# Optimization experiments

Hardware: AMD Instinct MI355X
Metric: run time of the kernel (lower is better)

Reference implementation:

```python
import jax, jax.numpy as jnp
import numpy as np

B, LE, LD = 8, 4096, 4096
DE, DD, A = 512, 512, 128


def setup_inputs() -> dict:
    key = jax.random.key(0)
    ks = jax.random.split(key, 9)
    f32 = jnp.float32
    return {
        "encoder_outputs": jax.random.normal(ks[0], (B, LE, DE), f32),
        "decoder_outputs": jax.random.normal(ks[1], (B, LD, DD), f32),
        # linear_q / linear_k / linear_v (Dense with bias, relu activation)
        "Wq": jax.random.normal(ks[2], (DD, A), f32) * 0.05,
        "bq": jnp.zeros((A,), f32),
        "Wk": jax.random.normal(ks[3], (DE, A), f32) * 0.05,
        "bk": jnp.zeros((A,), f32),
        "Wv": jax.random.normal(ks[4], (DE, A), f32) * 0.05,
        "bv": jnp.zeros((A,), f32),
        # perceptron branch weights (Dense, no bias)
        "Pw": jax.random.normal(ks[5], (A, A), f32) * 0.05,
        "Pu": jax.random.normal(ks[6], (A, A), f32) * 0.05,
        "pv": jax.random.normal(ks[7], (A, 1), f32) * 0.05,
    }


def reference(encoder_outputs, decoder_outputs, Wq, bq, Wk, bk, Wv, bv, Pw, Pu, pv):
    att = Wq.shape[1]
    q = jax.nn.relu(decoder_outputs @ Wq + bq)   # [B, Ld, A]
    k = jax.nn.relu(encoder_outputs @ Wk + bk)   # [B, Le, A]
    v = jax.nn.relu(encoder_outputs @ Wv + bv)   # [B, Le, A]
    # perceptron score: pv^T (Pw q_i + Pu k_j). No nonlinearity between the
    # sum and pv, so it decomposes additively -> no [B,Ld,Le,A] tiling needed.
    q_term = (q @ Pw) @ pv                        # [B, Ld, 1]
    k_term = (k @ Pu) @ pv                        # [B, Le, 1]
    scores = (q_term + jnp.swapaxes(k_term, 1, 2)) / jnp.sqrt(jnp.float32(att))  # [B, Ld, Le]
    weights = jax.nn.softmax(scores, axis=-1)
    attention = jnp.einsum('bij,bjd->bid', weights, v)  # [B, Ld, A]
    return attention
```

## Files before the change

kernel.cpp:

```cpp
#include <hip/hip_runtime.h>
#include <hip/hip_bf16.h>

#define B_   8
#define LE_  4096
#define LD_  4096
#define DE_  512
#define AA_  128
#define RTOT (B_*LE_)
#define NDIM 256
#define KDIM 512
#define BM   64
#define BK   64
#define LDSS 72

typedef __attribute__((ext_vector_type(8))) short short8;
typedef __attribute__((ext_vector_type(4))) float f32x4;

#define WCT_OFF   0
#define U_OFF     262144
#define BIAS_OFF  262656
#define NUM_OFF   263680
#define RS_OFF    267776
#define KT_OFF    267840
#define WW_OFF    398912
#define C_OFF     529984

__device__ inline ushort f2bf(float f) {
    union { float f; unsigned u; } x; x.f = f;
    unsigned r = x.u + 0x7fffu + ((x.u >> 16) & 1u);
    return (ushort)(r >> 16);
}

__global__ void prep_kernel(const float* __restrict__ Wk, const float* __restrict__ bk,
                            const float* __restrict__ Wv, const float* __restrict__ bv,
                            const float* __restrict__ Pu, const float* __restrict__ pv,
                            ushort* __restrict__ wct, float* __restrict__ u,
                            float* __restrict__ bias, float* __restrict__ num) {
    int t = threadIdx.x;
    int base = blockIdx.x * 256 + t;
    for (int i = 0; i < 4; ++i) {
        int idx = base + i * 32768;
        int n = idx >> 9, k = idx & 511;
        float s = (n < 128) ? Wk[k * 128 + n] : Wv[k * 128 + (n - 128)];
        wct[idx] = f2bf(s);
    }
    if (blockIdx.x == 0) {
        if (t < 128) {
            float acc = 0.f;
            for (int c = 0; c < 128; ++c) acc += Pu[t * 128 + c] * pv[c];
            u[t] = acc;
        }
        bias[t] = (t < 128) ? bk[t] : bv[t - 128];
        for (int i = 0; i < 4; ++i) num[t + i * 256] = 0.f;
    }
}

__global__ __launch_bounds__(256)
void gemm_kernel(const float* __restrict__ enc, const ushort* __restrict__ wct,
                 const float* __restrict__ bias, float* __restrict__ C) {
    __shared__ ushort As[BM][LDSS];
    __shared__ ushort Bs[NDIM][LDSS];
    const int t = threadIdx.x;
    const int wv = t >> 6, l = t & 63;
    const int m = l & 15, kb = l >> 4;
    const int row0 = blockIdx.x * BM;

    f32x4 acc[4][4] = {};

    for (int k0 = 0; k0 < KDIM; k0 += BK) {
#pragma unroll
        for (int i = 0; i < 2; ++i) {
            int c = t + i * 256;
            int r = c >> 3, k8 = (c & 7) * 8;
            const float4* src = (const float4*)(enc + (size_t)(row0 + r) * KDIM + k0 + k8);
            float4 a0 = src[0], a1 = src[1];
            int4 pk;
            pk.x = (int)f2bf(a0.x) | ((int)f2bf(a0.y) << 16);
            pk.y = (int)f2bf(a0.z) | ((int)f2bf(a0.w) << 16);
            pk.z = (int)f2bf(a1.x) | ((int)f2bf(a1.y) << 16);
            pk.w = (int)f2bf(a1.z) | ((int)f2bf(a1.w) << 16);
            *(int4*)&As[r][k8] = pk;
        }
#pragma unroll
        for (int i = 0; i < 8; ++i) {
            int c = t + i * 256;
            int n = c >> 3, k8 = (c & 7) * 8;
            int4 v = *(const int4*)(wct + (size_t)n * KDIM + k0 + k8);
            *(int4*)&Bs[n][k8] = v;
        }
        __syncthreads();
#pragma unroll
        for (int kc = 0; kc < 2; ++kc) {
            short8 afr[4], bfr[4];
#pragma unroll
            for (int mt = 0; mt < 4; ++mt)
                afr[mt] = *(const short8*)&As[mt * 16 + m][kc * 32 + kb * 8];
#pragma unroll
            for (int nt = 0; nt < 4; ++nt)
                bfr[nt] = *(const short8*)&Bs[wv * 64 + nt * 16 + m][kc * 32 + kb * 8];
#pragma unroll
            for (int mt = 0; mt < 4; ++mt)
#pragma unroll
                for (int nt = 0; nt < 4; ++nt)
                    acc[mt][nt] = __builtin_amdgcn_mfma_f32_16x16x32_bf16(
                        afr[mt], bfr[nt], acc[mt][nt], 0, 0, 0);
        }
        __syncthreads();
    }
    const int rgrp = l >> 4;
#pragma unroll
    for (int mt = 0; mt < 4; ++mt) {
#pragma unroll
        for (int nt = 0; nt < 4; ++nt) {
            int col = wv * 64 + nt * 16 + (l & 15);
            float bsv = bias[col];
#pragma unroll
            for (int r = 0; r < 4; ++r) {
                int rowl = mt * 16 + rgrp * 4 + r;
                float v = acc[mt][nt][r] + bsv;
                C[(size_t)(row0 + rowl) * NDIM + col] = v > 0.f ? v : 0.f;
            }
        }
    }
}

__global__ void kt_kernel(const float* __restrict__ C, const float* __restrict__ u,
                          float* __restrict__ kt) {
    int gid = blockIdx.x * 256 + threadIdx.x;
    int r = gid >> 6, l = gid & 63;
    float a = C[(size_t)r * NDIM + l] * u[l] + C[(size_t)r * NDIM + 64 + l] * u[64 + l];
#pragma unroll
    for (int off = 32; off > 0; off >>= 1) a += __shfl_down(a, off);
    if (l == 0) kt[r] = a;
}

__global__ __launch_bounds__(1024)
void softmax_kernel(const float* __restrict__ kt, float* __restrict__ w,
                    float* __restrict__ rS) {
    __shared__ float red[1024];
    int b = blockIdx.x, t = threadIdx.x;
    const float inv_s = 0.08838834764831843f;
    float v[4], m = -1e30f;
#pragma unroll
    for (int i = 0; i < 4; ++i) {
        v[i] = kt[b * 4096 + i * 1024 + t];
        m = fmaxf(m, v[i]);
    }
    red[t] = m; __syncthreads();
    for (int off = 512; off > 0; off >>= 1) {
        if (t < off) red[t] = fmaxf(red[t], red[t + off]);
        __syncthreads();
    }
    float M = red[0]; __syncthreads();
    float s = 0.f;
#pragma unroll
    for (int i = 0; i < 4; ++i) {
        float e = __expf((v[i] - M) * inv_s);
        w[b * 4096 + i * 1024 + t] = e;
        s += e;
    }
    red[t] = s; __syncthreads();
    for (int off = 512; off > 0; off >>= 1) {
        if (t < off) red[t] += red[t + off];
        __syncthreads();
    }
    if (t == 0) rS[b] = 1.0f / red[0];
}

__global__ void wsum_kernel(const float* __restrict__ C, const float* __restrict__ w,
                            float* __restrict__ num) {
    int b = blockIdx.x >> 4, ch = blockIdx.x & 15;
    int t = threadIdx.x;
    int d = t & 127, jj = t >> 7;
    size_t base_row = (size_t)b * 4096 + ch * 256;
    float acc = 0.f;
    for (int j = jj; j < 256; j += 2) {
        size_t r = base_row + j;
        acc += w[r] * C[r * NDIM + 128 + d];
    }
    atomicAdd(&num[b * 128 + d], acc);
}

__global__ void bcast_kernel(const float* __restrict__ num, const float* __restrict__ rS,
                             float4* __restrict__ out) {
    int g = blockIdx.x * 256 + threadIdx.x;
    const float4* n4 = (const float4*)num;
    const int total4 = B_ * LD_ * AA_ / 4;
    for (int c = g; c < total4; c += 262144) {
        int flat = c * 4;
        int b = flat >> 19;
        int d = flat & 127;
        float4 nv = n4[b * 32 + (d >> 2)];
        float s = rS[b];
        float4 o;
        o.x = nv.x * s; o.y = nv.y * s; o.z = nv.z * s; o.w = nv.w * s;
        out[c] = o;
    }
}

extern "C" void kernel_launch(void* const* d_in, const int* in_sizes, int n_in,
                              void* d_out, int out_size, void* d_ws, size_t ws_size,
                              hipStream_t stream) {
    const float* enc = (const float*)d_in[0];
    const float* Wk = (const float*)d_in[4];
    const float* bk = (const float*)d_in[5];
    const float* Wv = (const float*)d_in[6];
    const float* bv = (const float*)d_in[7];
    const float* Pu = (const float*)d_in[9];
    const float* pv = (const float*)d_in[10];

    char* ws = (char*)d_ws;
    ushort* wct  = (ushort*)(ws + WCT_OFF);
    float*  u    = (float*)(ws + U_OFF);
    float*  bias = (float*)(ws + BIAS_OFF);
    float*  num  = (float*)(ws + NUM_OFF);
    float*  rS   = (float*)(ws + RS_OFF);
    float*  kt   = (float*)(ws + KT_OFF);
    float*  w    = (float*)(ws + WW_OFF);
    float*  C    = (float*)(ws + C_OFF);

    prep_kernel<<<128, 256, 0, stream>>>(Wk, bk, Wv, bv, Pu, pv, wct, u, bias, num);
    gemm_kernel<<<RTOT / BM, 256, 0, stream>>>(enc, wct, bias, C);
    kt_kernel<<<RTOT / 4, 256, 0, stream>>>(C, u, kt);
    softmax_kernel<<<B_, 1024, 0, stream>>>(kt, w, rS);
    wsum_kernel<<<B_ * 16, 256, 0, stream>>>(C, w, num);
    bcast_kernel<<<1024, 256, 0, stream>>>(num, rS, (float4*)d_out);
}
```

Measured before the change: 214.0 us.

## Fuse key-score reduction into GEMM epilogue and store V as bf16

The GEMM now runs 512 threads per block with a 2x4 wave split. Its epilogue computes the k·u score directly using shuffle and LDS reductions, and writes only the V half, in bf16. This removes the kt kernel and the full fp32 C buffer round-trip through memory. Softmax now uses wave shuffles, normalizes the weights itself, and drops the separate reciprocal. wsum reads bf16 V with vectorized loads, and bcast becomes a pure copy. The cost is lower precision in V, which is rounded to bf16 before the weighted sum.

```diff
diff --git a/kernel.cpp b/kernel.cpp
--- a/kernel.cpp
+++ b/kernel.cpp
@@ -4,14 +4,10 @@
 #define B_   8
 #define LE_  4096
 #define LD_  4096
-#define DE_  512
+#define KDIM 512
 #define AA_  128
 #define RTOT (B_*LE_)
 #define NDIM 256
-#define KDIM 512
-#define BM   64
-#define BK   64
-#define LDSS 72
 
 typedef __attribute__((ext_vector_type(8))) short short8;
 typedef __attribute__((ext_vector_type(4))) float f32x4;
@@ -20,15 +16,18 @@
 #define U_OFF     262144
 #define BIAS_OFF  262656
 #define NUM_OFF   263680
-#define RS_OFF    267776
-#define KT_OFF    267840
-#define WW_OFF    398912
-#define C_OFF     529984
+#define S_OFF     267776
+#define WN_OFF    398848
+#define VB_OFF    529920
 
 __device__ inline ushort f2bf(float f) {
     union { float f; unsigned u; } x; x.f = f;
     unsigned r = x.u + 0x7fffu + ((x.u >> 16) & 1u);
     return (ushort)(r >> 16);
+}
+__device__ inline float bf2f(ushort s) {
+    union { unsigned u; float f; } x; x.u = ((unsigned)s) << 16;
+    return x.f;
 }
 
 __global__ void prep_kernel(const float* __restrict__ Wk, const float* __restrict__ bk,
@@ -55,23 +54,24 @@
     }
 }
 
-__global__ __launch_bounds__(256)
-void gemm_kernel(const float* __restrict__ enc, const ushort* __restrict__ wct,
-                 const float* __restrict__ bias, float* __restrict__ C) {
-    __shared__ ushort As[BM][LDSS];
-    __shared__ ushort Bs[NDIM][LDSS];
+__global__ __launch_bounds__(512, 4)
+void gemm_fused(const float* __restrict__ enc, const ushort* __restrict__ wct,
+                const float* __restrict__ bias, const float* __restrict__ u,
+                ushort* __restrict__ vbuf, float* __restrict__ sout) {
+    __shared__ ushort As[64][72];
+    __shared__ ushort Bs[256][72];
+    __shared__ float s_red[64][2];
     const int t = threadIdx.x;
     const int wv = t >> 6, l = t & 63;
+    const int wm = wv >> 2, wn = wv & 3;
     const int m = l & 15, kb = l >> 4;
-    const int row0 = blockIdx.x * BM;
-
-    f32x4 acc[4][4] = {};
-
-    for (int k0 = 0; k0 < KDIM; k0 += BK) {
-#pragma unroll
-        for (int i = 0; i < 2; ++i) {
-            int c = t + i * 256;
-            int r = c >> 3, k8 = (c & 7) * 8;
+    const int row0 = blockIdx.x * 64;
+
+    f32x4 acc[2][4] = {};
+
+    for (int k0 = 0; k0 < KDIM; k0 += 64) {
+        {
+            int r = t >> 3, k8 = (t & 7) * 8;
             const float4* src = (const float4*)(enc + (size_t)(row0 + r) * KDIM + k0 + k8);
             float4 a0 = src[0], a1 = src[1];
             int4 pk;
@@ -82,24 +82,23 @@
             *(int4*)&As[r][k8] = pk;
         }
 #pragma unroll
-        for (int i = 0; i < 8; ++i) {
-            int c = t + i * 256;
+        for (int i = 0; i < 4; ++i) {
+            int c = t + i * 512;
             int n = c >> 3, k8 = (c & 7) * 8;
-            int4 v = *(const int4*)(wct + (size_t)n * KDIM + k0 + k8);
-            *(int4*)&Bs[n][k8] = v;
+            *(int4*)&Bs[n][k8] = *(const int4*)(wct + (size_t)n * KDIM + k0 + k8);
         }
         __syncthreads();
 #pragma unroll
         for (int kc = 0; kc < 2; ++kc) {
-            short8 afr[4], bfr[4];
-#pragma unroll
-            for (int mt = 0; mt < 4; ++mt)
-                afr[mt] = *(const short8*)&As[mt * 16 + m][kc * 32 + kb * 8];
+            short8 afr[2], bfr[4];
+#pragma unroll
+            for (int mt = 0; mt < 2; ++mt)
+                afr[mt] = *(const short8*)&As[wm * 32 + mt * 16 + m][kc * 32 + kb * 8];
 #pragma unroll
             for (int nt = 0; nt < 4; ++nt)
-                bfr[nt] = *(const short8*)&Bs[wv * 64 + nt * 16 + m][kc * 32 + kb * 8];
-#pragma unroll
-            for (int mt = 0; mt < 4; ++mt)
+                bfr[nt] = *(const short8*)&Bs[wn * 64 + nt * 16 + m][kc * 32 + kb * 8];
+#pragma unroll
+            for (int mt = 0; mt < 2; ++mt)
 #pragma unroll
                 for (int nt = 0; nt < 4; ++nt)
                     acc[mt][nt] = __builtin_amdgcn_mfma_f32_16x16x32_bf16(
@@ -107,94 +106,141 @@
         }
         __syncthreads();
     }
-    const int rgrp = l >> 4;
-#pragma unroll
-    for (int mt = 0; mt < 4; ++mt) {
-#pragma unroll
-        for (int nt = 0; nt < 4; ++nt) {
-            int col = wv * 64 + nt * 16 + (l & 15);
-            float bsv = bias[col];
-#pragma unroll
-            for (int r = 0; r < 4; ++r) {
-                int rowl = mt * 16 + rgrp * 4 + r;
-                float v = acc[mt][nt][r] + bsv;
-                C[(size_t)(row0 + rowl) * NDIM + col] = v > 0.f ? v : 0.f;
-            }
-        }
-    }
-}
-
-__global__ void kt_kernel(const float* __restrict__ C, const float* __restrict__ u,
-                          float* __restrict__ kt) {
-    int gid = blockIdx.x * 256 + threadIdx.x;
-    int r = gid >> 6, l = gid & 63;
-    float a = C[(size_t)r * NDIM + l] * u[l] + C[(size_t)r * NDIM + 64 + l] * u[64 + l];
-#pragma unroll
-    for (int off = 32; off > 0; off >>= 1) a += __shfl_down(a, off);
-    if (l == 0) kt[r] = a;
+
+    const int rg = l >> 4;
+    if (wn >= 2) {
+#pragma unroll
+        for (int mt = 0; mt < 2; ++mt) {
+#pragma unroll
+            for (int nt = 0; nt < 4; ++nt) {
+                int col = wn * 64 + nt * 16 + m;
+                float bsv = bias[col];
+#pragma unroll
+                for (int j = 0; j < 4; ++j) {
+                    int rowl = wm * 32 + mt * 16 + rg * 4 + j;
+                    float v = acc[mt][nt][j] + bsv;
+                    v = v > 0.f ? v : 0.f;
+                    vbuf[(size_t)(row0 + rowl) * AA_ + (col - 128)] = f2bf(v);
+                }
+            }
+        }
+    } else {
+#pragma unroll
+        for (int mt = 0; mt < 2; ++mt) {
+            float p[4] = {0.f, 0.f, 0.f, 0.f};
+#pragma unroll
+            for (int nt = 0; nt < 4; ++nt) {
+                int col = wn * 64 + nt * 16 + m;
+                float bsv = bias[col];
+                float uw = u[col];
+#pragma unroll
+                for (int j = 0; j < 4; ++j) {
+                    float v = acc[mt][nt][j] + bsv;
+                    v = v > 0.f ? v : 0.f;
+                    p[j] += v * uw;
+                }
+            }
+#pragma unroll
+            for (int j = 0; j < 4; ++j) {
+                p[j] += __shfl_xor(p[j], 1);
+                p[j] += __shfl_xor(p[j], 2);
+                p[j] += __shfl_xor(p[j], 4);
+                p[j] += __shfl_xor(p[j], 8);
+            }
+            if (m == 0) {
+#pragma unroll
+                for (int j = 0; j < 4; ++j)
+                    s_red[wm * 32 + mt * 16 + rg * 4 + j][wn] = p[j];
+            }
+        }
+    }
+    __syncthreads();
+    if (t < 64) sout[row0 + t] = s_red[t][0] + s_red[t][1];
 }
 
 __global__ __launch_bounds__(1024)
-void softmax_kernel(const float* __restrict__ kt, float* __restrict__ w,
-                    float* __restrict__ rS) {
-    __shared__ float red[1024];
+void softmax_kernel(const float* __restrict__ s, float* __restrict__ wnorm) {
+    __shared__ float red[17];
     int b = blockIdx.x, t = threadIdx.x;
+    int l = t & 63, wv = t >> 6;
     const float inv_s = 0.08838834764831843f;
     float v[4], m = -1e30f;
 #pragma unroll
     for (int i = 0; i < 4; ++i) {
-        v[i] = kt[b * 4096 + i * 1024 + t];
+        v[i] = s[b * 4096 + i * 1024 + t];
         m = fmaxf(m, v[i]);
     }
-    red[t] = m; __syncthreads();
-    for (int off = 512; off > 0; off >>= 1) {
-        if (t < off) red[t] = fmaxf(red[t], red[t + off]);
-        __syncthreads();
-    }
-    float M = red[0]; __syncthreads();
-    float s = 0.f;
+#pragma unroll
+    for (int off = 1; off < 64; off <<= 1) m = fmaxf(m, __shfl_xor(m, off));
+    if (l == 0) red[wv] = m;
+    __syncthreads();
+    if (t == 0) {
+        float x = red[0];
+        for (int i = 1; i < 16; ++i) x = fmaxf(x, red[i]);
+        red[16] = x;
+    }
+    __syncthreads();
+    float M = red[16];
+    __syncthreads();
+    float e[4], sum = 0.f;
 #pragma unroll
     for (int i = 0; i < 4; ++i) {
-        float e = __expf((v[i] - M) * inv_s);
-        w[b * 4096 + i * 1024 + t] = e;
-        s += e;
-    }
-    red[t] = s; __syncthreads();
-    for (int off = 512; off > 0; off >>= 1) {
-        if (t < off) red[t] += red[t + off];
-        __syncthreads();
-    }
-    if (t == 0) rS[b] = 1.0f / red[0];
-}
-
-__global__ void wsum_kernel(const float* __restrict__ C, const float* __restrict__ w,
-                            float* __restrict__ num) {
-    int b = blockIdx.x >> 4, ch = blockIdx.x & 15;
-    int t = threadIdx.x;
-    int d = t & 127, jj = t >> 7;
-    size_t base_row = (size_t)b * 4096 + ch * 256;
-    float acc = 0.f;
-    for (int j = jj; j < 256; j += 2) {
-        size_t r = base_row + j;
-        acc += w[r] * C[r * NDIM + 128 + d];
-    }
-    atomicAdd(&num[b * 128 + d], acc);
-}
-
-__global__ void bcast_kernel(const float* __restrict__ num, const float* __restrict__ rS,
-                             float4* __restrict__ out) {
+        e[i] = __expf((v[i] - M) * inv_s);
+        sum += e[i];
+    }
+#pragma unroll
+    for (int off = 1; off < 64; off <<= 1) sum += __shfl_xor(sum, off);
+    if (l == 0) red[wv] = sum;
+    __syncthreads();
+    if (t == 0) {
+        float x = 0.f;
+        for (int i = 0; i < 16; ++i) x += red[i];
+        red[16] = 1.0f / x;
+    }
+    __syncthreads();
+    float rS = red[16];
+#pragma unroll
+    for (int i = 0; i < 4; ++i)
+        wnorm[b * 4096 + i * 1024 + t] = e[i] * rS;
+}
+
+__global__ __launch_bounds__(256)
+void wsum_kernel(const ushort* __restrict__ vbuf, const float* __restrict__ wnorm,
+                 float* __restrict__ num) {
+    int b = blockIdx.x >> 3, ch = blockIdx.x & 7;
+    int t = threadIdx.x, wv = t >> 6, l = t & 63;
+    int rg = l >> 4, d8 = (l & 15) * 8;
+    int rbase = b * 4096 + ch * 512;
+    float acc[8] = {};
+    for (int it = 0; it < 32; ++it) {
+        int r = rbase + it * 16 + wv * 4 + rg;
+        float wj = wnorm[r];
+        short8 vv = *(const short8*)(vbuf + (size_t)r * AA_ + d8);
+#pragma unroll
+        for (int j = 0; j < 8; ++j)
+            acc[j] += wj * bf2f((ushort)vv[j]);
+    }
+#pragma unroll
+    for (int j = 0; j < 8; ++j) {
+        acc[j] += __shfl_xor(acc[j], 16);
+        acc[j] += __shfl_xor(acc[j], 32);
+    }
+    if (l < 16) {
+#pragma unroll
+        for (int j = 0; j < 8; ++j)
+            atomicAdd(&num[b * AA_ + d8 + j], acc[j]);
+    }
+}
+
+__global__ void bcast_kernel(const float* __restrict__ num, float4* __restrict__ out) {
     int g = blockIdx.x * 256 + threadIdx.x;
     const float4* n4 = (const float4*)num;
     const int total4 = B_ * LD_ * AA_ / 4;
-    for (int c = g; c < total4; c += 262144) {
+    for (int c = g; c < total4; c += 524288) {
         int flat = c * 4;
         int b = flat >> 19;
         int d = flat & 127;
-        float4 nv = n4[b * 32 + (d >> 2)];
-        float s = rS[b];
-        float4 o;
-        o.x = nv.x * s; o.y = nv.y * s; o.z = nv.z * s; o.w = nv.w * s;
-        out[c] = o;
+        out[c] = n4[b * 32 + (d >> 2)];
     }
 }
 
@@ -210,19 +256,17 @@
     const float* pv = (const float*)d_in[10];
 
     char* ws = (char*)d_ws;
-    ushort* wct  = (ushort*)(ws + WCT_OFF);
-    float*  u    = (float*)(ws + U_OFF);
-    float*  bias = (float*)(ws + BIAS_OFF);
-    float*  num  = (float*)(ws + NUM_OFF);
-    float*  rS   = (float*)(ws + RS_OFF);
-    float*  kt   = (float*)(ws + KT_OFF);
-    float*  w    = (float*)(ws + WW_OFF);
-    float*  C    = (float*)(ws + C_OFF);
+    ushort* wct   = (ushort*)(ws + WCT_OFF);
+    float*  u     = (float*)(ws + U_OFF);
+    float*  bias  = (float*)(ws + BIAS_OFF);
+    float*  num   = (float*)(ws + NUM_OFF);
+    float*  s     = (float*)(ws + S_OFF);
+    float*  wnorm = (float*)(ws + WN_OFF);
+    ushort* vbuf  = (ushort*)(ws + VB_OFF);
 
     prep_kernel<<<128, 256, 0, stream>>>(Wk, bk, Wv, bv, Pu, pv, wct, u, bias, num);
-    gemm_kernel<<<RTOT / BM, 256, 0, stream>>>(enc, wct, bias, C);
-    kt_kernel<<<RTOT / 4, 256, 0, stream>>>(C, u, kt);
-    softmax_kernel<<<B_, 1024, 0, stream>>>(kt, w, rS);
-    wsum_kernel<<<B_ * 16, 256, 0, stream>>>(C, w, num);
-    bcast_kernel<<<1024, 256, 0, stream>>>(num, rS, (float4*)d_out);
-}
+    gemm_fused<<<RTOT / 64, 512, 0, stream>>>(enc, wct, bias, u, vbuf, s);
+    softmax_kernel<<<B_, 1024, 0, stream>>>(s, wnorm);
+    wsum_kernel<<<B_ * 8, 256, 0, stream>>>(vbuf, wnorm, num);
+    bcast_kernel<<<2048, 256, 0, stream>>>(num, (float4*)d_out);
+}
```

Result: faster. 184.1 us (-14.0%).
